# Performance work log

Measured on AMD Instinct MI355X. Metric: run time of the kernel, lower is better.

## Reference

```python
import jax, jax.numpy as jnp
import numpy as np

D_MODEL = 1024
N_HEAD = 16
B, S = 4, 1024


def setup_inputs() -> dict:
    key = jax.random.key(0)
    ks = jax.random.split(key, 10)
    f = lambda k, shp: jax.random.normal(k, shp, dtype=jnp.float32)
    return {
        "x": f(ks[0], (B, S, D_MODEL)),
        "y": f(ks[1], (B, S, D_MODEL)),
        "z": f(ks[2], (B, S, D_MODEL)),
        "mask": f(ks[3], (1, 1, S, S)) * 0.1,
        "wq_w": f(ks[4], (D_MODEL, D_MODEL)) * (D_MODEL ** -0.5),
        "wq_b": f(ks[5], (D_MODEL,)) * 0.02,
        "wk_w": f(ks[6], (D_MODEL, D_MODEL)) * (D_MODEL ** -0.5),
        "wk_b": f(ks[7], (D_MODEL,)) * 0.02,
        "wv_w": f(ks[8], (D_MODEL, D_MODEL)) * (D_MODEL ** -0.5),
        "wv_b": f(ks[9], (D_MODEL,)) * 0.02,
    }


def reference(x, y, z, mask, wq_w, wq_b, wk_w, wk_b, wv_w, wv_b):
    b, xl, d = x.shape
    hd = d // N_HEAD
    # linear projections (torch Linear: x @ W^T + b)
    q = x @ wq_w.T + wq_b
    k = y @ wk_w.T + wk_b
    v = z @ wv_w.T + wv_b
    # [B, H, L, hd]
    q = q.reshape(b, xl, N_HEAD, hd).transpose(0, 2, 1, 3)
    k = k.reshape(b, y.shape[1], N_HEAD, hd).transpose(0, 2, 1, 3)
    v = v.reshape(b, z.shape[1], N_HEAD, hd).transpose(0, 2, 1, 3)
    # NOTE: source scales by sqrt(d_model), not sqrt(head_dim)
    scale = 1.0 / jnp.sqrt(jnp.asarray(d, dtype=x.dtype))
    logits = jnp.einsum("bhqd,bhkd->bhqk", q, k) * scale
    score = jax.nn.softmax(logits, axis=-1)
    # mask added AFTER softmax (faithful to source)
    score = score + mask
    out = jnp.einsum("bhqk,bhkd->bhqd", score, v)
    return out.transpose(0, 2, 1, 3).reshape(b, xl, d)
```

## Files before the change

kernel.cpp:

```cpp
#include <hip/hip_runtime.h>
#include <hip/hip_bf16.h>
#include <cstdint>

typedef __bf16 bf16_t;
typedef __bf16 bf16x8 __attribute__((ext_vector_type(8)));
typedef __bf16 bf16x4 __attribute__((ext_vector_type(4)));
typedef float floatx4 __attribute__((ext_vector_type(4)));

typedef __attribute__((address_space(3))) uint32_t lds_u32_t;
typedef const __attribute__((address_space(1))) uint32_t g_u32_t;

#define MFMA_BF16(a, b, c) __builtin_amdgcn_mfma_f32_16x16x32_bf16((a), (b), (c), 0, 0, 0)

static constexpr int S = 1024;
static constexpr int HD = 64;

struct ConvArgs {
  const float* src[7];
  bf16_t* dst[7];
  int n[7];
};

__global__ __launch_bounds__(256) void convert_kernel(ConvArgs a) {
  const int j = blockIdx.y;
  const float4* __restrict__ s = (const float4*)a.src[j];
  bf16x4* __restrict__ d = (bf16x4*)a.dst[j];
  const int n4 = a.n[j] >> 2;
  for (int i = blockIdx.x * blockDim.x + threadIdx.x; i < n4; i += gridDim.x * blockDim.x) {
    float4 v = s[i];
    bf16x4 o;
    o[0] = (bf16_t)v.x; o[1] = (bf16_t)v.y; o[2] = (bf16_t)v.z; o[3] = (bf16_t)v.w;
    d[i] = o;
  }
}

struct GemmCfg {
  const bf16_t* A;
  const bf16_t* Bm;
  void* out;
  const float* bias;
  int mode;
};

union GemmSmem {
  struct { bf16_t A[128 * 64]; bf16_t B[128 * 64]; } ab;
  bf16_t C[128 * 136];
};

__global__ __launch_bounds__(256, 3) void gemm_nt_kernel(GemmCfg c0, GemmCfg c1, GemmCfg c2, int K) {
  GemmCfg cfg = (blockIdx.y == 0) ? c0 : (blockIdx.y == 1 ? c1 : c2);
  __shared__ GemmSmem u;
  __shared__ float bias_s[128];
  const int tid = threadIdx.x;
  const int wave = tid >> 6;
  const int lane = tid & 63;
  const int g = lane >> 4;
  const int cl = lane & 15;
  const int mq = (wave & 1) * 64;
  const int nq = (wave >> 1) * 64;

  const int xcd = blockIdx.x & 7, idx = blockIdx.x >> 3;
  int mb, nb;
  if (cfg.mode == 0) { mb = xcd * 4 + (idx & 3); nb = idx >> 2; }
  else               { nb = xcd * 4 + (idx & 3); mb = idx >> 2; }
  const int m0 = mb * 128, n0 = nb * 128;

  if (tid < 128) bias_s[tid] = cfg.bias[(cfg.mode == 0 ? n0 : m0) + tid];

  const int srow = tid >> 3;
  const int sch = (tid & 7) ^ (srow & 7);
  const bf16_t* Ag = cfg.A + (size_t)(m0 + srow) * K + sch * 8;
  const bf16_t* Bg = cfg.Bm + (size_t)(n0 + srow) * K + sch * 8;
  const int swz = cl & 7;

  floatx4 acc[4][4];
#pragma unroll
  for (int i = 0; i < 4; ++i)
#pragma unroll
    for (int j = 0; j < 4; ++j) acc[i][j] = floatx4{0.f, 0.f, 0.f, 0.f};

  const int kiters = K >> 6;
  for (int kt = 0; kt < kiters; ++kt) {
    __syncthreads();
#pragma unroll
    for (int i = 0; i < 4; ++i) {
      __builtin_amdgcn_global_load_lds((g_u32_t*)(const void*)(Ag + (size_t)(i * 32) * K),
                                       (lds_u32_t*)(void*)&u.ab.A[(i * 256 + tid) * 8], 16, 0, 0);
      __builtin_amdgcn_global_load_lds((g_u32_t*)(const void*)(Bg + (size_t)(i * 32) * K),
                                       (lds_u32_t*)(void*)&u.ab.B[(i * 256 + tid) * 8], 16, 0, 0);
    }
    Ag += 64;
    Bg += 64;
    __syncthreads();

#pragma unroll
    for (int kc = 0; kc < 2; ++kc) {
      bf16x8 af[4], bfr[4];
#pragma unroll
      for (int i = 0; i < 4; ++i)
        af[i] = *(const bf16x8*)&u.ab.A[(mq + i * 16 + cl) * 64 + ((kc * 4 + g) ^ swz) * 8];
#pragma unroll
      for (int j = 0; j < 4; ++j)
        bfr[j] = *(const bf16x8*)&u.ab.B[(nq + j * 16 + cl) * 64 + ((kc * 4 + g) ^ swz) * 8];
#pragma unroll
      for (int i = 0; i < 4; ++i)
#pragma unroll
        for (int j = 0; j < 4; ++j) acc[i][j] = MFMA_BF16(af[i], bfr[j], acc[i][j]);
    }
  }

  __syncthreads();
#pragma unroll
  for (int i = 0; i < 4; ++i)
#pragma unroll
    for (int j = 0; j < 4; ++j)
#pragma unroll
      for (int r = 0; r < 4; ++r) {
        const int ml = mq + i * 16 + g * 4 + r;
        const int nl = nq + j * 16 + cl;
        float v = acc[i][j][r] + bias_s[cfg.mode == 0 ? nl : ml];
        u.C[ml * 136 + nl] = (bf16_t)v;
      }
  __syncthreads();
#pragma unroll
  for (int it = 0; it < 8; ++it) {
    const int ix = it * 256 + tid;
    const int ml = ix >> 4, nc = ix & 15;
    bf16x8 val = *(const bf16x8*)&u.C[ml * 136 + nc * 8];
    const int m = m0 + ml, n = n0 + nc * 8;
    size_t addr;
    if (cfg.mode == 0)
      addr = (size_t)((m >> 10) * 16 + (n >> 6)) * 65536 + (m & 1023) * 64 + (n & 63);
    else
      addr = (size_t)((n >> 10) * 16 + (m >> 6)) * 65536 + (m & 63) * 1024 + (n & 1023);
    *(bf16x8*)&((bf16_t*)cfg.out)[addr] = val;
  }
}

__global__ __launch_bounds__(256, 2) void attn_kernel(const bf16_t* __restrict__ Q,
                                                      const bf16_t* __restrict__ Kb,
                                                      const bf16_t* __restrict__ Vt,
                                                      const bf16_t* __restrict__ Mk,
                                                      float* __restrict__ out) {
  __shared__ bf16_t Ks[128 * 64];
  __shared__ bf16_t Vs[64 * 128];
  __shared__ bf16_t Pbuf[4][32 * 136];
  const int tid = threadIdx.x;
  const int wave = tid >> 6, lane = tid & 63;
  const int g = lane >> 4, cl = lane & 15;
  const int bh = blockIdx.x & 63, qt = blockIdx.x >> 6;
  const int q0w = qt * 128 + wave * 32;
  const bf16_t* Qp = Q + (size_t)bh * (S * HD);
  const bf16_t* Kp = Kb + (size_t)bh * (S * HD);
  const bf16_t* Vp = Vt + (size_t)bh * (S * HD);
  bf16_t* Pw = &Pbuf[wave][0];

  const int krow = tid >> 3, kch = (tid & 7) ^ (krow & 7);
  const int vrow = tid >> 4, vch = (tid & 15) ^ (vrow & 7);
  const int sw = cl & 7;

  bf16x8 qf[2][2];
#pragma unroll
  for (int nj = 0; nj < 2; ++nj)
#pragma unroll
    for (int kc = 0; kc < 2; ++kc)
      qf[nj][kc] = *(const bf16x8*)&Qp[(size_t)(q0w + nj * 16 + cl) * HD + kc * 32 + g * 8];

  floatx4 o[2][4], o2[2][4];
#pragma unroll
  for (int mi = 0; mi < 2; ++mi)
#pragma unroll
    for (int nj = 0; nj < 4; ++nj) {
      o[mi][nj] = floatx4{0.f, 0.f, 0.f, 0.f};
      o2[mi][nj] = floatx4{0.f, 0.f, 0.f, 0.f};
    }
  float dsq[2] = {0.f, 0.f};

  for (int kt = 0; kt < 8; ++kt) {
    const int k0 = kt * 128;
    __syncthreads();
#pragma unroll
    for (int i = 0; i < 4; ++i)
      __builtin_amdgcn_global_load_lds(
          (g_u32_t*)(const void*)&Kp[(size_t)(k0 + i * 32 + krow) * HD + kch * 8],
          (lds_u32_t*)(void*)&Ks[(i * 256 + tid) * 8], 16, 0, 0);
#pragma unroll
    for (int i = 0; i < 4; ++i)
      __builtin_amdgcn_global_load_lds(
          (g_u32_t*)(const void*)&Vp[(size_t)(i * 16 + vrow) * S + k0 + vch * 8],
          (lds_u32_t*)(void*)&Vs[(i * 256 + tid) * 8], 16, 0, 0);
    __syncthreads();

#pragma unroll
    for (int mi = 0; mi < 8; ++mi) {
      bf16x8 kf0 = *(const bf16x8*)&Ks[(mi * 16 + cl) * 64 + ((0 + g) ^ sw) * 8];
      bf16x8 kf1 = *(const bf16x8*)&Ks[(mi * 16 + cl) * 64 + ((4 + g) ^ sw) * 8];
      floatx4 s0 = floatx4{0.f, 0.f, 0.f, 0.f}, s1 = floatx4{0.f, 0.f, 0.f, 0.f};
      s0 = MFMA_BF16(kf0, qf[0][0], s0);
      s0 = MFMA_BF16(kf1, qf[0][1], s0);
      s1 = MFMA_BF16(kf0, qf[1][0], s1);
      s1 = MFMA_BF16(kf1, qf[1][1], s1);
      bf16x4 p0, p1;
#pragma unroll
      for (int r = 0; r < 4; ++r) {
        float e0 = __expf(s0[r] * 0.03125f);
        float e1 = __expf(s1[r] * 0.03125f);
        dsq[0] += e0;
        dsq[1] += e1;
        p0[r] = (bf16_t)e0;
        p1[r] = (bf16_t)e1;
      }
      *(bf16x4*)&Pw[(cl)*136 + mi * 16 + g * 4] = p0;
      *(bf16x4*)&Pw[(16 + cl) * 136 + mi * 16 + g * 4] = p1;
    }

#pragma unroll
    for (int kc = 0; kc < 4; ++kc) {
      bf16x8 pa0 = *(const bf16x8*)&Pw[cl * 136 + kc * 32 + g * 8];
      bf16x8 pa1 = *(const bf16x8*)&Pw[(16 + cl) * 136 + kc * 32 + g * 8];
      bf16x8 ma0 = *(const bf16x8*)&Mk[(size_t)(q0w + cl) * S + k0 + kc * 32 + g * 8];
      bf16x8 ma1 = *(const bf16x8*)&Mk[(size_t)(q0w + 16 + cl) * S + k0 + kc * 32 + g * 8];
#pragma unroll
      for (int nj = 0; nj < 4; ++nj) {
        bf16x8 vf = *(const bf16x8*)&Vs[(nj * 16 + cl) * 128 + ((kc * 4 + g) ^ sw) * 8];
        o[0][nj] = MFMA_BF16(pa0, vf, o[0][nj]);
        o[1][nj] = MFMA_BF16(pa1, vf, o[1][nj]);
        o2[0][nj] = MFMA_BF16(ma0, vf, o2[0][nj]);
        o2[1][nj] = MFMA_BF16(ma1, vf, o2[1][nj]);
      }
    }
  }

#pragma unroll
  for (int nj = 0; nj < 2; ++nj) {
    dsq[nj] += __shfl_xor(dsq[nj], 16, 64);
    dsq[nj] += __shfl_xor(dsq[nj], 32, 64);
  }

  const int b = bh >> 4, h = bh & 15;
#pragma unroll
  for (int mi = 0; mi < 2; ++mi) {
#pragma unroll
    for (int r = 0; r < 4; ++r) {
      float dv = __shfl(dsq[mi], g * 4 + r, 64);
      float dinv = 1.0f / dv;
      const int srow = q0w + mi * 16 + g * 4 + r;
#pragma unroll
      for (int nj = 0; nj < 4; ++nj) {
        const int hd = nj * 16 + cl;
        out[((size_t)b * S + srow) * 1024 + h * HD + hd] = o[mi][nj][r] * dinv + o2[mi][nj][r];
      }
    }
  }
}

extern "C" void kernel_launch(void* const* d_in, const int* in_sizes, int n_in,
                              void* d_out, int out_size, void* d_ws, size_t ws_size,
                              hipStream_t stream) {
  const float* x = (const float*)d_in[0];
  const float* y = (const float*)d_in[1];
  const float* z = (const float*)d_in[2];
  const float* mask = (const float*)d_in[3];
  const float* wq_w = (const float*)d_in[4];
  const float* wq_b = (const float*)d_in[5];
  const float* wk_w = (const float*)d_in[6];
  const float* wk_b = (const float*)d_in[7];
  const float* wv_w = (const float*)d_in[8];
  const float* wv_b = (const float*)d_in[9];

  uint8_t* ws = (uint8_t*)d_ws;
  const size_t MB = 1u << 20;
  bf16_t* Xb = (bf16_t*)(ws + 0 * MB);
  bf16_t* Yb = (bf16_t*)(ws + 8 * MB);
  bf16_t* Zb = (bf16_t*)(ws + 16 * MB);
  bf16_t* Wqb = (bf16_t*)(ws + 24 * MB);
  bf16_t* Wkb = (bf16_t*)(ws + 26 * MB);
  bf16_t* Wvb = (bf16_t*)(ws + 28 * MB);
  bf16_t* Mb = (bf16_t*)(ws + 30 * MB);
  bf16_t* Qb = (bf16_t*)(ws + 32 * MB);
  bf16_t* Kb = (bf16_t*)(ws + 40 * MB);
  bf16_t* Vtb = (bf16_t*)(ws + 48 * MB);

  ConvArgs ca;
  ca.src[0] = x;    ca.dst[0] = Xb;  ca.n[0] = 4 * 1024 * 1024;
  ca.src[1] = y;    ca.dst[1] = Yb;  ca.n[1] = 4 * 1024 * 1024;
  ca.src[2] = z;    ca.dst[2] = Zb;  ca.n[2] = 4 * 1024 * 1024;
  ca.src[3] = wq_w; ca.dst[3] = Wqb; ca.n[3] = 1024 * 1024;
  ca.src[4] = wk_w; ca.dst[4] = Wkb; ca.n[4] = 1024 * 1024;
  ca.src[5] = wv_w; ca.dst[5] = Wvb; ca.n[5] = 1024 * 1024;
  ca.src[6] = mask; ca.dst[6] = Mb;  ca.n[6] = 1024 * 1024;
  convert_kernel<<<dim3(512, 7), 256, 0, stream>>>(ca);

  GemmCfg cq{Xb, Wqb, (void*)Qb, wq_b, 0};
  GemmCfg ck{Yb, Wkb, (void*)Kb, wk_b, 0};
  GemmCfg cv{Wvb, Zb, (void*)Vtb, wv_b, 1};
  gemm_nt_kernel<<<dim3(256, 3), 256, 0, stream>>>(cq, ck, cv, 1024);

  attn_kernel<<<dim3(512), 256, 0, stream>>>(Qb, Kb, Vtb, Mb, (float*)d_out);
}
```

Before: 176.7 us.

## Shrink attention tiles to 16 query rows per wave and 64-key chunks

Each wave in the attention kernel now handles 16 query rows instead of 32, and each block covers 64 queries, which doubles the grid to 1024 blocks. Keys and values are staged in 64-key tiles (16 iterations) instead of 128. Launch bounds request 4 blocks per CU. The aim is more occupancy and smaller register and LDS footprints to hide latency, at the cost of loading K/V from global memory twice as often per query and more barriers.

Result: slower. 186.3 us (+5.4%).

```diff
diff --git a/kernel.cpp b/kernel.cpp
--- a/kernel.cpp
+++ b/kernel.cpp
@@ -137,119 +137,103 @@
   }
 }
 
-__global__ __launch_bounds__(256, 2) void attn_kernel(const bf16_t* __restrict__ Q,
+__global__ __launch_bounds__(256, 4) void attn_kernel(const bf16_t* __restrict__ Q,
                                                       const bf16_t* __restrict__ Kb,
                                                       const bf16_t* __restrict__ Vt,
                                                       const bf16_t* __restrict__ Mk,
                                                       float* __restrict__ out) {
-  __shared__ bf16_t Ks[128 * 64];
-  __shared__ bf16_t Vs[64 * 128];
-  __shared__ bf16_t Pbuf[4][32 * 136];
+  __shared__ bf16_t Ks[64 * 64];
+  __shared__ bf16_t Vs[64 * 64];
+  __shared__ bf16_t Pbuf[4][16 * 72];
   const int tid = threadIdx.x;
   const int wave = tid >> 6, lane = tid & 63;
   const int g = lane >> 4, cl = lane & 15;
   const int bh = blockIdx.x & 63, qt = blockIdx.x >> 6;
-  const int q0w = qt * 128 + wave * 32;
+  const int q0w = qt * 64 + wave * 16;
   const bf16_t* Qp = Q + (size_t)bh * (S * HD);
   const bf16_t* Kp = Kb + (size_t)bh * (S * HD);
   const bf16_t* Vp = Vt + (size_t)bh * (S * HD);
   bf16_t* Pw = &Pbuf[wave][0];
 
-  const int krow = tid >> 3, kch = (tid & 7) ^ (krow & 7);
-  const int vrow = tid >> 4, vch = (tid & 15) ^ (vrow & 7);
+  const int srow = tid >> 3, sch = (tid & 7) ^ ((tid >> 3) & 7);
   const int sw = cl & 7;
 
-  bf16x8 qf[2][2];
-#pragma unroll
-  for (int nj = 0; nj < 2; ++nj)
+  bf16x8 qf[2];
+#pragma unroll
+  for (int kc = 0; kc < 2; ++kc)
+    qf[kc] = *(const bf16x8*)&Qp[(size_t)(q0w + cl) * HD + kc * 32 + g * 8];
+
+  floatx4 o[4], o2[4];
+#pragma unroll
+  for (int nj = 0; nj < 4; ++nj) {
+    o[nj] = floatx4{0.f, 0.f, 0.f, 0.f};
+    o2[nj] = floatx4{0.f, 0.f, 0.f, 0.f};
+  }
+  float dsq = 0.f;
+
+  for (int kt = 0; kt < 16; ++kt) {
+    const int k0 = kt * 64;
+
+    bf16x8 ma[2];
 #pragma unroll
     for (int kc = 0; kc < 2; ++kc)
-      qf[nj][kc] = *(const bf16x8*)&Qp[(size_t)(q0w + nj * 16 + cl) * HD + kc * 32 + g * 8];
-
-  floatx4 o[2][4], o2[2][4];
-#pragma unroll
-  for (int mi = 0; mi < 2; ++mi)
-#pragma unroll
-    for (int nj = 0; nj < 4; ++nj) {
-      o[mi][nj] = floatx4{0.f, 0.f, 0.f, 0.f};
-      o2[mi][nj] = floatx4{0.f, 0.f, 0.f, 0.f};
-    }
-  float dsq[2] = {0.f, 0.f};
-
-  for (int kt = 0; kt < 8; ++kt) {
-    const int k0 = kt * 128;
-    __syncthreads();
-#pragma unroll
-    for (int i = 0; i < 4; ++i)
+      ma[kc] = *(const bf16x8*)&Mk[(size_t)(q0w + cl) * S + k0 + kc * 32 + g * 8];
+
+    __syncthreads();
+#pragma unroll
+    for (int i = 0; i < 2; ++i)
       __builtin_amdgcn_global_load_lds(
-          (g_u32_t*)(const void*)&Kp[(size_t)(k0 + i * 32 + krow) * HD + kch * 8],
+          (g_u32_t*)(const void*)&Kp[(size_t)(k0 + i * 32 + srow) * HD + sch * 8],
           (lds_u32_t*)(void*)&Ks[(i * 256 + tid) * 8], 16, 0, 0);
 #pragma unroll
-    for (int i = 0; i < 4; ++i)
+    for (int i = 0; i < 2; ++i)
       __builtin_amdgcn_global_load_lds(
-          (g_u32_t*)(const void*)&Vp[(size_t)(i * 16 + vrow) * S + k0 + vch * 8],
+          (g_u32_t*)(const void*)&Vp[(size_t)(i * 32 + srow) * S + k0 + sch * 8],
           (lds_u32_t*)(void*)&Vs[(i * 256 + tid) * 8], 16, 0, 0);
     __syncthreads();
 
 #pragma unroll
-    for (int mi = 0; mi < 8; ++mi) {
+    for (int mi = 0; mi < 4; ++mi) {
       bf16x8 kf0 = *(const bf16x8*)&Ks[(mi * 16 + cl) * 64 + ((0 + g) ^ sw) * 8];
       bf16x8 kf1 = *(const bf16x8*)&Ks[(mi * 16 + cl) * 64 + ((4 + g) ^ sw) * 8];
-      floatx4 s0 = floatx4{0.f, 0.f, 0.f, 0.f}, s1 = floatx4{0.f, 0.f, 0.f, 0.f};
-      s0 = MFMA_BF16(kf0, qf[0][0], s0);
-      s0 = MFMA_BF16(kf1, qf[0][1], s0);
-      s1 = MFMA_BF16(kf0, qf[1][0], s1);
-      s1 = MFMA_BF16(kf1, qf[1][1], s1);
-      bf16x4 p0, p1;
+      floatx4 s0 = floatx4{0.f, 0.f, 0.f, 0.f};
+      s0 = MFMA_BF16(kf0, qf[0], s0);
+      s0 = MFMA_BF16(kf1, qf[1], s0);
+      bf16x4 p0;
 #pragma unroll
       for (int r = 0; r < 4; ++r) {
         float e0 = __expf(s0[r] * 0.03125f);
-        float e1 = __expf(s1[r] * 0.03125f);
-        dsq[0] += e0;
-        dsq[1] += e1;
+        dsq += e0;
         p0[r] = (bf16_t)e0;
-        p1[r] = (bf16_t)e1;
       }
-      *(bf16x4*)&Pw[(cl)*136 + mi * 16 + g * 4] = p0;
-      *(bf16x4*)&Pw[(16 + cl) * 136 + mi * 16 + g * 4] = p1;
-    }
-
-#pragma unroll
-    for (int kc = 0; kc < 4; ++kc) {
-      bf16x8 pa0 = *(const bf16x8*)&Pw[cl * 136 + kc * 32 + g * 8];
-      bf16x8 pa1 = *(const bf16x8*)&Pw[(16 + cl) * 136 + kc * 32 + g * 8];
-      bf16x8 ma0 = *(const bf16x8*)&Mk[(size_t)(q0w + cl) * S + k0 + kc * 32 + g * 8];
-      bf16x8 ma1 = *(const bf16x8*)&Mk[(size_t)(q0w + 16 + cl) * S + k0 + kc * 32 + g * 8];
+      *(bf16x4*)&Pw[cl * 72 + mi * 16 + g * 4] = p0;
+    }
+
+#pragma unroll
+    for (int kc = 0; kc < 2; ++kc) {
+      bf16x8 pa = *(const bf16x8*)&Pw[cl * 72 + kc * 32 + g * 8];
 #pragma unroll
       for (int nj = 0; nj < 4; ++nj) {
-        bf16x8 vf = *(const bf16x8*)&Vs[(nj * 16 + cl) * 128 + ((kc * 4 + g) ^ sw) * 8];
-        o[0][nj] = MFMA_BF16(pa0, vf, o[0][nj]);
-        o[1][nj] = MFMA_BF16(pa1, vf, o[1][nj]);
-        o2[0][nj] = MFMA_BF16(ma0, vf, o2[0][nj]);
-        o2[1][nj] = MFMA_BF16(ma1, vf, o2[1][nj]);
+        bf16x8 vf = *(const bf16x8*)&Vs[(nj * 16 + cl) * 64 + ((kc * 4 + g) ^ sw) * 8];
+        o[nj] = MFMA_BF16(pa, vf, o[nj]);
+        o2[nj] = MFMA_BF16(ma[kc], vf, o2[nj]);
       }
     }
   }
 
-#pragma unroll
-  for (int nj = 0; nj < 2; ++nj) {
-    dsq[nj] += __shfl_xor(dsq[nj], 16, 64);
-    dsq[nj] += __shfl_xor(dsq[nj], 32, 64);
-  }
+  dsq += __shfl_xor(dsq, 16, 64);
+  dsq += __shfl_xor(dsq, 32, 64);
 
   const int b = bh >> 4, h = bh & 15;
 #pragma unroll
-  for (int mi = 0; mi < 2; ++mi) {
-#pragma unroll
-    for (int r = 0; r < 4; ++r) {
-      float dv = __shfl(dsq[mi], g * 4 + r, 64);
-      float dinv = 1.0f / dv;
-      const int srow = q0w + mi * 16 + g * 4 + r;
-#pragma unroll
-      for (int nj = 0; nj < 4; ++nj) {
-        const int hd = nj * 16 + cl;
-        out[((size_t)b * S + srow) * 1024 + h * HD + hd] = o[mi][nj][r] * dinv + o2[mi][nj][r];
-      }
+  for (int r = 0; r < 4; ++r) {
+    float dv = __shfl(dsq, g * 4 + r, 64);
+    float dinv = 1.0f / dv;
+    const int orow = q0w + g * 4 + r;
+#pragma unroll
+    for (int nj = 0; nj < 4; ++nj) {
+      const int hd = nj * 16 + cl;
+      out[((size_t)b * S + orow) * 1024 + h * HD + hd] = o[nj][r] * dinv + o2[nj][r];
     }
   }
 }
@@ -296,5 +280,5 @@
   GemmCfg cv{Wvb, Zb, (void*)Vtb, wv_b, 1};
   gemm_nt_kernel<<<dim3(256, 3), 256, 0, stream>>>(cq, ck, cv, 1024);
 
-  attn_kernel<<<dim3(512), 256, 0, stream>>>(Qb, Kb, Vtb, Mb, (float*)d_out);
-}
+  attn_kernel<<<dim3(1024), 256, 0, stream>>>(Qb, Kb, Vtb, Mb, (float*)d_out);
+}
```
